# Performance work log

Hardware: AMD Instinct MI355X
Metric: run time of the kernel (lower is better)

## Reference

```python
import jax, jax.numpy as jnp
import numpy as np

KCONV = 4
NSTATE = 64
NH_SPA = 4
NH_SPE = 8
NH_ATTN = 8
QLEN = 5


def _ln(x, w, b, eps=1e-5):
    mu = jnp.mean(x, -1, keepdims=True)
    var = jnp.var(x, -1, keepdims=True)
    return (x - mu) * jax.lax.rsqrt(var + eps) * w + b


def _sincos_2d(dim, H):
    # standard 2D sin-cos positional embedding, [H*H, dim]
    def e1(d, pos):
        omega = 1.0 / (10000.0 ** (np.arange(d // 2, dtype=np.float64) / (d / 2.0)))
        out = pos[:, None] * omega[None, :]
        return np.concatenate([np.sin(out), np.cos(out)], axis=-1)
    gh, gw = np.meshgrid(np.arange(H), np.arange(H), indexing='ij')
    emb = np.concatenate([e1(dim // 2, gh.reshape(-1)), e1(dim // 2, gw.reshape(-1))], axis=-1)
    return jnp.asarray(emb, jnp.float32)


def _ssd_scan(x, dt, A, Bm, Cm):
    # x:[b,l,h,p] dt:[b,l,h] A:[h] Bm,Cm:[b,l,n] (ngroups=1)
    b, l, h, p = x.shape
    dA = jnp.exp(dt * A)            # [b,l,h]
    dtx = dt[..., None] * x          # [b,l,h,p]

    def step(hs, inp):
        dA_t, dtx_t, B_t, C_t = inp
        hs = hs * dA_t[:, :, None, None] + dtx_t[..., None] * B_t[:, None, None, :]
        return hs, jnp.einsum('bhpn,bn->bhp', hs, C_t)

    h0 = jnp.zeros((b, h, p, Bm.shape[-1]), x.dtype)
    _, ys = jax.lax.scan(step, h0, (dA.transpose(1, 0, 2), dtx.transpose(1, 0, 2, 3),
                                    Bm.transpose(1, 0, 2), Cm.transpose(1, 0, 2)))
    return ys.transpose(1, 0, 2, 3)


def _mamba2(u, in_w, conv_w, conv_b, dt_bias, A_log, Dp, rms_w, out_w, nheads, n=NSTATE):
    # Mamba2 forward (d_state=64, d_conv=4, expand=2, rmsnorm gated, no biases on projections)
    b, l, _ = u.shape
    d_in_proj = in_w.shape[0]
    d_inner = (d_in_proj - 2 * n - nheads) // 2
    zxbcdt = u @ in_w.T
    z = zxbcdt[..., :d_inner]
    xBC = zxbcdt[..., d_inner:2 * d_inner + 2 * n]
    dt = jax.nn.softplus(zxbcdt[..., 2 * d_inner + 2 * n:] + dt_bias)  # [b,l,h]
    # causal depthwise conv1d, kernel 4
    xp = jnp.pad(xBC, ((0, 0), (KCONV - 1, 0), (0, 0)))
    xc = sum(xp[:, k:k + l, :] * conv_w[:, k] for k in range(KCONV)) + conv_b
    xBC = jax.nn.silu(xc)
    xh = xBC[..., :d_inner].reshape(b, l, nheads, -1)
    Bm = xBC[..., d_inner:d_inner + n]
    Cm = xBC[..., d_inner + n:]
    y = _ssd_scan(xh, dt, -jnp.exp(A_log), Bm, Cm)
    y = y + Dp[None, None, :, None] * xh
    y = y.reshape(b, l, -1) * jax.nn.silu(z)
    y = y * jax.lax.rsqrt(jnp.mean(y * y, -1, keepdims=True) + 1e-5) * rms_w
    return y @ out_w.T


def _forward(floats, sorted_index):
    (x, spa_ln_w, spa_ln_b, spa_in_w, spa_conv_w, spa_conv_b, spa_dt_bias, spa_A_log, spa_D,
     spa_rms_w, spa_out_w, spe_ln_w, spe_ln_b, spe_in_w, spe_conv_w, spe_conv_b, spe_dt_bias,
     spe_A_log, spe_D, spe_rms_w, spe_out_w, norm_w, norm_b, cprj_w, cprj_b,
     aq_w, aq_b, ak_w, ak_b, av_w, av_b, ao_w, ao_b,
     sq_w, sq_b, sk_w, sk_b, sv_w, sv_b, so_w, so_b,
     ds_conv_w, ds_ln_w, ds_ln_b) = floats
    b, c, H, W = x.shape
    # seq_generate: pos embed + reorder by (precomputed MST/BFS) sorted_index
    pe = _sincos_2d(c, H)                                  # [H*W, c]
    xs = x.transpose(0, 2, 3, 1).reshape(b, H * W, c) + pe[None]
    xs = jnp.take_along_axis(xs, sorted_index[..., None], axis=1)
    # SSD blocks
    for i in range(spa_ln_w.shape[0]):
        h1 = _mamba2(_ln(xs, spa_ln_w[i], spa_ln_b[i]), spa_in_w[i], spa_conv_w[i], spa_conv_b[i],
                     spa_dt_bias[i], spa_A_log[i], spa_D[i], spa_rms_w[i], spa_out_w[i], NH_SPA) + xs
        h2 = _mamba2(_ln(h1.transpose(0, 2, 1), spe_ln_w[i], spe_ln_b[i]), spe_in_w[i], spe_conv_w[i],
                     spe_conv_b[i], spe_dt_bias[i], spe_A_log[i], spe_D[i], spe_rms_w[i], spe_out_w[i], NH_SPE)
        xs = h2.transpose(0, 2, 1) + h1
    xs = _ln(xs, norm_w, norm_b)
    # center query: Conv1d(kernel=QLEN, pad=0) over the first QLEN tokens -> [b, c]
    center = jnp.einsum('blc,ocl->bo', xs[:, :QLEN, :], cprj_w) + cprj_b
    # Spa_Attention: center query attends over all tokens; per-token reweighting of V
    nh = NH_ATTN
    hd = c // nh
    q = (center @ aq_w.T + aq_b).reshape(b, nh, hd)
    k = (xs @ ak_w.T + ak_b).reshape(b, -1, nh, hd)
    v = (xs @ av_w.T + av_b).reshape(b, -1, nh, hd)
    attn = jax.nn.softmax(jnp.einsum('bhd,blhd->bhl', q, k) / float(np.sqrt(hd)), axis=-1)
    out = (v * attn.transpose(0, 2, 1)[..., None]).reshape(b, -1, c) @ ao_w.T + ao_b
    xs = xs + out
    # Spe_Attention: self-attention over channel tokens (dim = seq_len)
    xt = xs.transpose(0, 2, 1)                              # [b, c, L]
    q2 = xt @ sq_w.T + sq_b
    k2 = xt @ sk_w.T + sk_b
    v2 = xt @ sv_w.T + sv_b
    attn2 = jax.nn.softmax(jnp.einsum('bqd,bkd->bqk', q2, k2) / float(np.sqrt(xt.shape[-1])), axis=-1)
    xs = xs + ((attn2 @ v2) @ so_w.T + so_b).transpose(0, 2, 1)
    # Downsample: invert ordering, reshape to image, conv stride 2, LayerNorm
    inv = jnp.argsort(sorted_index, axis=1)
    xr = jnp.take_along_axis(xs, inv[..., None], axis=1).reshape(b, H, W, c)
    y = jax.lax.conv_general_dilated(xr, ds_conv_w, (2, 2), [(1, 1), (1, 1)],
                                     dimension_numbers=('NHWC', 'HWIO', 'NHWC'))
    return _ln(y, ds_ln_w, ds_ln_b)  # [b, H/2, W/2, c]


def setup_inputs() -> dict:
    key = jax.random.key(0)
    ks = iter(jax.random.split(key, 64))

    def rn(shape, s=0.02):
        return jax.random.normal(next(ks), shape, jnp.float32) * s

    d = {}
    d['x'] = jax.random.normal(next(ks), (16, 128, 16, 16), jnp.float32)
    d['sorted_index'] = jnp.argsort(jax.random.uniform(next(ks), (16, 256)), axis=1)
    d['spa_ln_w'] = jnp.ones((2, 128), jnp.float32)
    d['spa_ln_b'] = jnp.zeros((2, 128), jnp.float32)
    d['spa_in_w'] = rn((2, 644, 128))
    d['spa_conv_w'] = rn((2, 384, 4), 0.2)
    d['spa_conv_b'] = jnp.zeros((2, 384), jnp.float32)
    d['spa_dt_bias'] = rn((2, 4), 0.1) - 2.0
    d['spa_A_log'] = jnp.log(jax.random.uniform(next(ks), (2, 4), minval=1.0, maxval=8.0))
    d['spa_D'] = jnp.ones((2, 4), jnp.float32)
    d['spa_rms_w'] = jnp.ones((2, 256), jnp.float32)
    d['spa_out_w'] = rn((2, 128, 256))
    d['spe_ln_w'] = jnp.ones((2, 256), jnp.float32)
    d['spe_ln_b'] = jnp.zeros((2, 256), jnp.float32)
    d['spe_in_w'] = rn((2, 1160, 256))
    d['spe_conv_w'] = rn((2, 640, 4), 0.2)
    d['spe_conv_b'] = jnp.zeros((2, 640), jnp.float32)
    d['spe_dt_bias'] = rn((2, 8), 0.1) - 2.0
    d['spe_A_log'] = jnp.log(jax.random.uniform(next(ks), (2, 8), minval=1.0, maxval=8.0))
    d['spe_D'] = jnp.ones((2, 8), jnp.float32)
    d['spe_rms_w'] = jnp.ones((2, 512), jnp.float32)
    d['spe_out_w'] = rn((2, 256, 512))
    d['norm_w'] = jnp.ones((128,), jnp.float32)
    d['norm_b'] = jnp.zeros((128,), jnp.float32)
    d['cprj_w'] = rn((128, 128, 5), 0.05)
    d['cprj_b'] = jnp.zeros((128,), jnp.float32)
    for nm in ['aq', 'ak', 'av', 'ao']:
        d[nm + '_w'] = rn((128, 128), 0.05)
        d[nm + '_b'] = jnp.zeros((128,), jnp.float32)
    for nm in ['sq', 'sk', 'sv', 'so']:
        d[nm + '_w'] = rn((256, 256), 0.05)
        d[nm + '_b'] = jnp.zeros((256,), jnp.float32)
    d['ds_conv_w'] = rn((3, 3, 128, 128), 0.05)
    d['ds_ln_w'] = jnp.ones((128,), jnp.float32)
    d['ds_ln_b'] = jnp.zeros((128,), jnp.float32)
    return d


def reference(x, sorted_index, spa_ln_w, spa_ln_b, spa_in_w, spa_conv_w, spa_conv_b, spa_dt_bias,
              spa_A_log, spa_D, spa_rms_w, spa_out_w, spe_ln_w, spe_ln_b, spe_in_w, spe_conv_w,
              spe_conv_b, spe_dt_bias, spe_A_log, spe_D, spe_rms_w, spe_out_w, norm_w, norm_b,
              cprj_w, cprj_b, aq_w, aq_b, ak_w, ak_b, av_w, av_b, ao_w, ao_b,
              sq_w, sq_b, sk_w, sk_b, sv_w, sv_b, so_w, so_b, ds_conv_w, ds_ln_w, ds_ln_b):
    floats = (x, spa_ln_w, spa_ln_b, spa_in_w, spa_conv_w, spa_conv_b, spa_dt_bias, spa_A_log, spa_D,
              spa_rms_w, spa_out_w, spe_ln_w, spe_ln_b, spe_in_w, spe_conv_w, spe_conv_b, spe_dt_bias,
              spe_A_log, spe_D, spe_rms_w, spe_out_w, norm_w, norm_b, cprj_w, cprj_b,
              aq_w, aq_b, ak_w, ak_b, av_w, av_b, ao_w, ao_b,
              sq_w, sq_b, sk_w, sk_b, sv_w, sv_b, so_w, so_b, ds_conv_w, ds_ln_w, ds_ln_b)
    return _forward(floats, sorted_index)
```

## Files before the change

kernel.cpp:

```cpp
#include <hip/hip_runtime.h>
#include <math.h>

#define DEV __device__ __forceinline__

typedef __attribute__((ext_vector_type(8))) short short8;
typedef __attribute__((ext_vector_type(4))) float f32x4;
typedef unsigned short ushort_t;
typedef unsigned int uint_t;

DEV float siluf(float x){ return x / (1.f + __expf(-x)); }
DEV float softplusf(float x){ return (x > 20.f) ? x : log1pf(__expf(x)); }

DEV ushort_t bf16r(float f){
    uint_t u = __float_as_uint(f);
    return (ushort_t)((u + 0x7fffu + ((u >> 16) & 1u)) >> 16);
}
DEV uint_t pack2(float a, float b){
    return (uint_t)bf16r(a) | ((uint_t)bf16r(b) << 16);
}

DEV void blk_sum2(float &a, float &b, float* sm){
    int lane = threadIdx.x & 63, wid = threadIdx.x >> 6, nw = blockDim.x >> 6;
    #pragma unroll
    for (int off = 32; off; off >>= 1){ a += __shfl_down(a, off); b += __shfl_down(b, off); }
    if (lane == 0){ sm[wid] = a; sm[8 + wid] = b; }
    __syncthreads();
    float ra = 0.f, rb = 0.f;
    for (int i = 0; i < nw; i++){ ra += sm[i]; rb += sm[8 + i]; }
    __syncthreads();
    a = ra; b = rb;
}
DEV float blk_sum1(float v, float* sm){
    int lane = threadIdx.x & 63, wid = threadIdx.x >> 6, nw = blockDim.x >> 6;
    #pragma unroll
    for (int off = 32; off; off >>= 1) v += __shfl_down(v, off);
    if (lane == 0) sm[wid] = v;
    __syncthreads();
    float r = 0.f;
    for (int i = 0; i < nw; i++) r += sm[i];
    __syncthreads();
    return r;
}
DEV float blk_max1(float v, float* sm){
    int lane = threadIdx.x & 63, wid = threadIdx.x >> 6, nw = blockDim.x >> 6;
    #pragma unroll
    for (int off = 32; off; off >>= 1) v = fmaxf(v, __shfl_down(v, off));
    if (lane == 0) sm[wid] = v;
    __syncthreads();
    float r = -3.4e38f;
    for (int i = 0; i < nw; i++) r = fmaxf(r, sm[i]);
    __syncthreads();
    return r;
}

DEV void tr_body(const float* __restrict__ ip, float* __restrict__ op,
                 int R, int C, int c0, int r0){
    __shared__ float tile[32][33];
    int tx = threadIdx.x & 31, ty = threadIdx.x >> 5;
    #pragma unroll
    for (int rr = ty; rr < 32; rr += 8)
        tile[rr][tx] = ip[(size_t)(r0 + rr) * C + c0 + tx];
    __syncthreads();
    #pragma unroll
    for (int rr = ty; rr < 32; rr += 8)
        op[(size_t)(c0 + rr) * R + r0 + tx] = tile[tx][rr];
}

__global__ __launch_bounds__(256) void k_tr(const float* __restrict__ in,
                                            float* __restrict__ out, int R, int C){
    tr_body(in + (size_t)blockIdx.z * R * C, out + (size_t)blockIdx.z * R * C,
            R, C, blockIdx.x * 32, blockIdx.y * 32);
}

__global__ __launch_bounds__(256) void k_tr_multi(const float* __restrict__ x,
        float* __restrict__ xT, const float* __restrict__ aow, float* __restrict__ owt,
        const float* __restrict__ sow, float* __restrict__ sowt){
    int idx = blockIdx.x;
    if (idx < 512){
        int bx = idx & 7, by = (idx >> 3) & 3, bz = idx >> 5;
        tr_body(x + (size_t)bz * 32768, xT + (size_t)bz * 32768, 128, 256, bx * 32, by * 32);
    } else if (idx < 528){
        int l = idx - 512;
        tr_body(aow, owt, 128, 128, (l & 3) * 32, (l >> 2) * 32);
    } else {
        int l = idx - 528;
        tr_body(sow, sowt, 256, 256, (l & 7) * 32, (l >> 3) * 32);
    }
}

__global__ void k_embed(const float* __restrict__ xT, const int* __restrict__ sidx,
                        float* __restrict__ xs){
    int bl = blockIdx.x; int b = bl >> 8; int c = threadIdx.x;
    int p = sidx[bl];
    int hh = p >> 4, ww = p & 15;
    int pos = (c < 64) ? hh : ww;
    int jm = c & 63;
    float om = __expf(-(float)(jm & 31) * 0.28782313662425574f);
    float ang = (float)pos * om;
    float pe = (jm < 32) ? sinf(ang) : cosf(ang);
    xs[(size_t)bl * 128 + c] = xT[((size_t)(b * 256 + p)) * 128 + c] + pe;
}

__global__ void k_ln(const float* __restrict__ in, const float* __restrict__ w,
                     const float* __restrict__ bb, float* __restrict__ out, int dim){
    __shared__ float sm[16];
    int row = blockIdx.x, t = threadIdx.x;
    float v = in[(size_t)row * dim + t];
    float a = v, q = v * v;
    blk_sum2(a, q, sm);
    float inv = 1.f / (float)dim;
    float mu = a * inv;
    float var = q * inv - mu * mu;
    float rs = rsqrtf(var + 1e-5f);
    out[(size_t)row * dim + t] = (v - mu) * rs * w[t] + bb[t];
}


__global__ __launch_bounds__(256) void k_gemm_ln(const float* __restrict__ A,
        const float* __restrict__ W, const float* __restrict__ lw,
        const float* __restrict__ lb, float* __restrict__ out, int N, int K){
    __shared__ __align__(16) ushort_t smem[2 * 64 * 72];
    ushort_t (*Abf)[72] = (ushort_t (*)[72])smem;
    ushort_t (*Wbf)[72] = (ushort_t (*)[72])(smem + 64 * 72);
    int j0 = blockIdx.x * 64, r0 = blockIdx.y * 64;
    int tid = threadIdx.x;
    int row = tid >> 2, kg = tid & 3;
    int wrow = j0 + row; if (wrow > N - 1) wrow = N - 1;
    const float* Ar = A + (size_t)(r0 + row) * K;
    const float* Wr = W + (size_t)wrow * K;
    float s = 0.f, ss = 0.f;
    for (int k0 = 0; k0 < K; k0 += 32){
        float4 a0 = *(const float4*)(Ar + k0 + kg * 4);
        float4 a1 = *(const float4*)(Ar + k0 + 16 + kg * 4);
        s  += a0.x + a0.y + a0.z + a0.w + a1.x + a1.y + a1.z + a1.w;
        ss += a0.x*a0.x + a0.y*a0.y + a0.z*a0.z + a0.w*a0.w
            + a1.x*a1.x + a1.y*a1.y + a1.z*a1.z + a1.w*a1.w;
    }
    s  += __shfl_xor(s, 1);  ss += __shfl_xor(ss, 1);
    s  += __shfl_xor(s, 2);  ss += __shfl_xor(ss, 2);
    float inv = 1.f / (float)K;
    float mu = s * inv;
    float rs = rsqrtf(ss * inv - mu * mu + 1e-5f);
    int wv = tid >> 6, lane = tid & 63, lm = lane & 15, quad = lane >> 4;
    f32x4 zero4 = {0.f, 0.f, 0.f, 0.f};
    f32x4 acc[4] = {zero4, zero4, zero4, zero4};
    for (int kc0 = 0; kc0 < K; kc0 += 64){
        int kb = kc0 + kg * 16;
        float4 q[4], g[4], b[4], p[4];
        #pragma unroll
        for (int i = 0; i < 4; i++){
            q[i] = *(const float4*)(Ar + kb + i * 4);
            g[i] = *(const float4*)(lw + kb + i * 4);
            b[i] = *(const float4*)(lb + kb + i * 4);
            p[i] = *(const float4*)(Wr + kb + i * 4);
        }
        #pragma unroll
        for (int i = 0; i < 4; i++){
            q[i].x = (q[i].x - mu) * rs * g[i].x + b[i].x;
            q[i].y = (q[i].y - mu) * rs * g[i].y + b[i].y;
            q[i].z = (q[i].z - mu) * rs * g[i].z + b[i].z;
            q[i].w = (q[i].w - mu) * rs * g[i].w + b[i].w;
        }
        __syncthreads();
        {
            uint4 u0, u1;
            u0.x = pack2(q[0].x, q[0].y); u0.y = pack2(q[0].z, q[0].w);
            u0.z = pack2(q[1].x, q[1].y); u0.w = pack2(q[1].z, q[1].w);
            u1.x = pack2(q[2].x, q[2].y); u1.y = pack2(q[2].z, q[2].w);
            u1.z = pack2(q[3].x, q[3].y); u1.w = pack2(q[3].z, q[3].w);
            *(uint4*)&Abf[row][kg * 16] = u0;
            *(uint4*)&Abf[row][kg * 16 + 8] = u1;
            u0.x = pack2(p[0].x, p[0].y); u0.y = pack2(p[0].z, p[0].w);
            u0.z = pack2(p[1].x, p[1].y); u0.w = pack2(p[1].z, p[1].w);
            u1.x = pack2(p[2].x, p[2].y); u1.y = pack2(p[2].z, p[2].w);
            u1.z = pack2(p[3].x, p[3].y); u1.w = pack2(p[3].z, p[3].w);
            *(uint4*)&Wbf[row][kg * 16] = u0;
            *(uint4*)&Wbf[row][kg * 16 + 8] = u1;
        }
        __syncthreads();
        #pragma unroll
        for (int kk = 0; kk < 64; kk += 32){
            short8 af = *(const short8*)&Abf[wv * 16 + lm][kk + quad * 8];
            #pragma unroll
            for (int c = 0; c < 4; c++){
                short8 bfv = *(const short8*)&Wbf[c * 16 + lm][kk + quad * 8];
                acc[c] = __builtin_amdgcn_mfma_f32_16x16x32_bf16(af, bfv, acc[c], 0, 0, 0);
            }
        }
    }
    int rbase = r0 + wv * 16 + quad * 4;
    #pragma unroll
    for (int c = 0; c < 4; c++){
        int j = j0 + c * 16 + lm;
        if (j < N){
            #pragma unroll
            for (int reg = 0; reg < 4; reg++)
                out[(size_t)(rbase + reg) * N + j] = acc[c][reg];
        }
    }
}

__global__ __launch_bounds__(256) void k_gemm_gate(const float* __restrict__ Y,
        const float* __restrict__ Z, const float* __restrict__ rw,
        const float* __restrict__ W, const float* __restrict__ res,
        float* __restrict__ out, int N, int K, int zs, int mode){
    __shared__ __align__(16) ushort_t smem[2 * 64 * 72];
    ushort_t (*Abf)[72] = (ushort_t (*)[72])smem;
    ushort_t (*Wbf)[72] = (ushort_t (*)[72])(smem + 64 * 72);
    __shared__ float sscale[64];
    int j0 = blockIdx.x * 64, r0 = blockIdx.y * 64;
    int tid = threadIdx.x;
    int row = tid >> 2, kg = tid & 3;
    const float* Yr = Y + (size_t)(r0 + row) * K;
    const float* Zr = Z + (size_t)(r0 + row) * zs;
    const float* Wr = W + (size_t)(j0 + row) * K;
    int wv = tid >> 6, lane = tid & 63, lm = lane & 15, quad = lane >> 4;
    float ssq = 0.f;
    f32x4 zero4 = {0.f, 0.f, 0.f, 0.f};
    f32x4 acc[4] = {zero4, zero4, zero4, zero4};
    for (int kc0 = 0; kc0 < K; kc0 += 64){
        int kb = kc0 + kg * 16;
        float4 y[4], z[4], g[4], p[4];
        #pragma unroll
        for (int i = 0; i < 4; i++){
            y[i] = *(const float4*)(Yr + kb + i * 4);
            z[i] = *(const float4*)(Zr + kb + i * 4);
            g[i] = *(const float4*)(rw + kb + i * 4);
            p[i] = *(const float4*)(Wr + kb + i * 4);
        }
        #pragma unroll
        for (int i = 0; i < 4; i++){
            y[i].x *= siluf(z[i].x); y[i].y *= siluf(z[i].y);
            y[i].z *= siluf(z[i].z); y[i].w *= siluf(z[i].w);
            ssq += y[i].x*y[i].x + y[i].y*y[i].y + y[i].z*y[i].z + y[i].w*y[i].w;
            y[i].x *= g[i].x; y[i].y *= g[i].y; y[i].z *= g[i].z; y[i].w *= g[i].w;
        }
        __syncthreads();
        {
            uint4 u0, u1;
            u0.x = pack2(y[0].x, y[0].y); u0.y = pack2(y[0].z, y[0].w);
            u0.z = pack2(y[1].x, y[1].y); u0.w = pack2(y[1].z, y[1].w);
            u1.x = pack2(y[2].x, y[2].y); u1.y = pack2(y[2].z, y[2].w);
            u1.z = pack2(y[3].x, y[3].y); u1.w = pack2(y[3].z, y[3].w);
            *(uint4*)&Abf[row][kg * 16] = u0;
            *(uint4*)&Abf[row][kg * 16 + 8] = u1;
            u0.x = pack2(p[0].x, p[0].y); u0.y = pack2(p[0].z, p[0].w);
            u0.z = pack2(p[1].x, p[1].y); u0.w = pack2(p[1].z, p[1].w);
            u1.x = pack2(p[2].x, p[2].y); u1.y = pack2(p[2].z, p[2].w);
            u1.z = pack2(p[3].x, p[3].y); u1.w = pack2(p[3].z, p[3].w);
            *(uint4*)&Wbf[row][kg * 16] = u0;
            *(uint4*)&Wbf[row][kg * 16 + 8] = u1;
        }
        __syncthreads();
        #pragma unroll
        for (int kk = 0; kk < 64; kk += 32){
            short8 af = *(const short8*)&Abf[wv * 16 + lm][kk + quad * 8];
            #pragma unroll
            for (int c = 0; c < 4; c++){
                short8 bfv = *(const short8*)&Wbf[c * 16 + lm][kk + quad * 8];
                acc[c] = __builtin_amdgcn_mfma_f32_16x16x32_bf16(af, bfv, acc[c], 0, 0, 0);
            }
        }
    }
    ssq += __shfl_xor(ssq, 1);
    ssq += __shfl_xor(ssq, 2);
    if (kg == 0) sscale[row] = rsqrtf(ssq / (float)K + 1e-5f);
    __syncthreads();
    int lr0 = wv * 16 + quad * 4;
    float scr[4];
    #pragma unroll
    for (int reg = 0; reg < 4; reg++) scr[reg] = sscale[lr0 + reg];
    if (mode == 2){
        float (*T)[68] = (float (*)[68])smem;
        #pragma unroll
        for (int c = 0; c < 4; c++)
            #pragma unroll
            for (int reg = 0; reg < 4; reg++)
                T[c * 16 + lm][lr0 + reg] = acc[c][reg] * scr[reg];
        __syncthreads();
        int b2 = r0 >> 7, ii0 = r0 & 127;
        int jj = tid >> 2, seg = tid & 3;
        size_t base = ((size_t)(b2 * 256 + j0 + jj)) * 128 + ii0 + seg * 16;
        float* op = out + base;
        const float* rp = res + base;
        #pragma unroll
        for (int c = 0; c < 4; c++){
            float4 v = *(const float4*)(&T[jj][seg * 16 + c * 4]);
            float4 rv = *(const float4*)(rp + c * 4);
            v.x += rv.x; v.y += rv.y; v.z += rv.z; v.w += rv.w;
            *(float4*)(op + c * 4) = v;
        }
    } else {
        int rbase = r0 + lr0;
        #pragma unroll
        for (int c = 0; c < 4; c++){
            int j = j0 + c * 16 + lm;
            #pragma unroll
            for (int reg = 0; reg < 4; reg++){
                size_t oi = (size_t)(rbase + reg) * N + j;
                out[oi] = acc[c][reg] * scr[reg] + res[oi];
            }
        }
    }
}

struct GJob { const float* W; const float* bias; float* out; int mode; };

__global__ __launch_bounds__(256) void k_gemm3(const float* __restrict__ A,
                                               GJob ja, GJob jb, GJob jc,
                                               int N, int K){
    GJob job = (blockIdx.z == 0) ? ja : ((blockIdx.z == 1) ? jb : jc);
    const float* W = job.W;
    const float* bias = job.bias;
    float* out = job.out;
    int mode = job.mode;
    __shared__ __align__(16) ushort_t smem[2 * 64 * 72];
    ushort_t (*Abf)[72] = (ushort_t (*)[72])smem;
    ushort_t (*Wbf)[72] = (ushort_t (*)[72])(smem + 64 * 72);
    int j0 = blockIdx.x * 64, r0 = blockIdx.y * 64;
    int tid = threadIdx.x;
    int row = tid >> 2, kg = tid & 3;
    const float* Ar = A + (size_t)(r0 + row) * K;
    const float* Wr = W + (size_t)(j0 + row) * K;
    int wv = tid >> 6, lane = tid & 63, lm = lane & 15, quad = lane >> 4;
    f32x4 zero4 = {0.f, 0.f, 0.f, 0.f};
    f32x4 acc[4] = {zero4, zero4, zero4, zero4};
    for (int kc0 = 0; kc0 < K; kc0 += 64){
        int kb = kc0 + kg * 16;
        float4 q[4], p[4];
        #pragma unroll
        for (int i = 0; i < 4; i++){
            q[i] = *(const float4*)(Ar + kb + i * 4);
            p[i] = *(const float4*)(Wr + kb + i * 4);
        }
        __syncthreads();
        {
            uint4 u0, u1;
            u0.x = pack2(q[0].x, q[0].y); u0.y = pack2(q[0].z, q[0].w);
            u0.z = pack2(q[1].x, q[1].y); u0.w = pack2(q[1].z, q[1].w);
            u1.x = pack2(q[2].x, q[2].y); u1.y = pack2(q[2].z, q[2].w);
            u1.z = pack2(q[3].x, q[3].y); u1.w = pack2(q[3].z, q[3].w);
            *(uint4*)&Abf[row][kg * 16] = u0;
            *(uint4*)&Abf[row][kg * 16 + 8] = u1;
            u0.x = pack2(p[0].x, p[0].y); u0.y = pack2(p[0].z, p[0].w);
            u0.z = pack2(p[1].x, p[1].y); u0.w = pack2(p[1].z, p[1].w);
            u1.x = pack2(p[2].x, p[2].y); u1.y = pack2(p[2].z, p[2].w);
            u1.z = pack2(p[3].x, p[3].y); u1.w = pack2(p[3].z, p[3].w);
            *(uint4*)&Wbf[row][kg * 16] = u0;
            *(uint4*)&Wbf[row][kg * 16 + 8] = u1;
        }
        __syncthreads();
        #pragma unroll
        for (int kk = 0; kk < 64; kk += 32){
            short8 af = *(const short8*)&Abf[wv * 16 + lm][kk + quad * 8];
            #pragma unroll
            for (int c = 0; c < 4; c++){
                short8 bfv = *(const short8*)&Wbf[c * 16 + lm][kk + quad * 8];
                acc[c] = __builtin_amdgcn_mfma_f32_16x16x32_bf16(af, bfv, acc[c], 0, 0, 0);
            }
        }
    }
    int lr0 = wv * 16 + quad * 4;
    if (mode == 3){
        __syncthreads();
        float (*T)[68] = (float (*)[68])smem;
        #pragma unroll
        for (int c = 0; c < 4; c++)
            #pragma unroll
            for (int reg = 0; reg < 4; reg++)
                T[c * 16 + lm][lr0 + reg] = acc[c][reg];
        __syncthreads();
        int b2 = r0 >> 7, ii0 = r0 & 127;
        int jj = tid >> 2, seg = tid & 3;
        size_t base = ((size_t)(b2 * 256 + j0 + jj)) * 128 + ii0 + seg * 16;
        float* op = out + base;
        float bj = bias[j0 + jj];
        #pragma unroll
        for (int c = 0; c < 4; c++){
            float4 v = *(const float4*)(&T[jj][seg * 16 + c * 4]);
            v.x += bj; v.y += bj; v.z += bj; v.w += bj;
            *(float4*)(op + c * 4) = v;
        }
    } else {
        int rbase = r0 + lr0;
        #pragma unroll
        for (int c = 0; c < 4; c++){
            int j = j0 + c * 16 + lm;
            float bj = bias[j];
            #pragma unroll
            for (int reg = 0; reg < 4; reg++)
                out[(size_t)(rbase + reg) * N + j] = acc[c][reg] + bj;
        }
    }
}

__global__ void k_conv(const float* __restrict__ zx, const float* __restrict__ cw,
                       const float* __restrict__ cb, float* __restrict__ xc,
                       const float* __restrict__ dtbias, const float* __restrict__ Al,
                       float* __restrict__ dt, float* __restrict__ dlA,
                       int L, int D, int stride, int off, int nh, int dtoff){
    int bl = blockIdx.x;
    int l = bl & (L - 1);
    const float* base = zx + (size_t)bl * stride + off;
    for (int d = threadIdx.x; d < D; d += blockDim.x){
        float acc = cb[d];
        #pragma unroll
        for (int k = 0; k < 4; k++){
            int dl = l + k - 3;
            if (dl >= 0) acc += base[(ptrdiff_t)(k - 3) * stride + d] * cw[d * 4 + k];
        }
        xc[(size_t)bl * D + d] = siluf(acc);
    }
    int t = threadIdx.x;
    if (t < nh){
        float xv = zx[(size_t)bl * stride + dtoff + t] + dtbias[t];
        float d = softplusf(xv);
        dt[(size_t)bl * nh + t] = d;
        dlA[(size_t)bl * nh + t] = -d * __expf(Al[t]);
    }
}

__global__ __launch_bounds__(256) void k_ssd_chunk(
        const float* __restrict__ xc, const float* __restrict__ dt,
        const float* __restrict__ dlA, float* __restrict__ y,
        float* __restrict__ S, float* __restrict__ clb,
        int L, int nh, int nc, int xcs, int bo, int co, int ys){
    __shared__ float sX[64][68];
    __shared__ float sB[64][68];
    __shared__ float sC[64][68];
    __shared__ float cl[64], sdt[64], sw[64];
    int blk = blockIdx.x;
    int c = blk % nc; int bh = blk / nc; int h = bh % nh; int b = bh / nh;
    int l0 = c * 64;
    int tid = threadIdx.x;
    const float* base = xc + ((size_t)(b * L + l0)) * xcs;
    for (int idx = tid; idx < 4096; idx += 256){
        int s = idx >> 6, n = idx & 63;
        const float* row = base + (size_t)s * xcs;
        sX[s][n] = row[h * 64 + n];
        sB[s][n] = row[bo + n];
        sC[s][n] = row[co + n];
    }
    if (tid < 64){
        size_t di = (size_t)(b * L + l0 + tid) * nh + h;
        float dlv = dlA[di];
        sdt[tid] = dt[di];
        #pragma unroll
        for (int off = 1; off < 64; off <<= 1){
            float o = __shfl_up(dlv, off, 64);
            if (tid >= off) dlv += o;
        }
        cl[tid] = dlv;
        clb[(size_t)blk * 64 + tid] = dlv;
    }
    __syncthreads();
    if (tid < 64) sw[tid] = __expf(cl[63] - cl[tid]) * sdt[tid];

    int g1 = tid >> 4, g2 = tid & 15;
    int t0 = g1 * 4, s0 = g2 * 4;
    float g[4][4] = {};
    for (int n = 0; n < 64; n += 4){
        float4 cv[4], bv[4];
        #pragma unroll
        for (int i = 0; i < 4; i++) cv[i] = *(const float4*)&sC[t0 + i][n];
        #pragma unroll
        for (int j = 0; j < 4; j++) bv[j] = *(const float4*)&sB[s0 + j][n];
        #pragma unroll
        for (int i = 0; i < 4; i++)
            #pragma unroll
            for (int j = 0; j < 4; j++){
                g[i][j] = fmaf(cv[i].x, bv[j].x, g[i][j]);
                g[i][j] = fmaf(cv[i].y, bv[j].y, g[i][j]);
                g[i][j] = fmaf(cv[i].z, bv[j].z, g[i][j]);
                g[i][j] = fmaf(cv[i].w, bv[j].w, g[i][j]);
            }
    }
    __syncthreads();
    #pragma unroll
    for (int i = 0; i < 4; i++)
        #pragma unroll
        for (int j = 0; j < 4; j++){
            int t = t0 + i, s = s0 + j;
            float v = 0.f;
            if (s <= t) v = g[i][j] * __expf(cl[t] - cl[s]) * sdt[s];
            sC[t][s] = v;
        }
    __syncthreads();
    {
        float acc[4][4] = {};
        for (int s = 0; s < 64; s++){
            float4 xv = *(const float4*)&sX[s][s0];
            float gv[4];
            #pragma unroll
            for (int i = 0; i < 4; i++) gv[i] = sC[t0 + i][s];
            #pragma unroll
            for (int i = 0; i < 4; i++){
                acc[i][0] = fmaf(gv[i], xv.x, acc[i][0]);
                acc[i][1] = fmaf(gv[i], xv.y, acc[i][1]);
                acc[i][2] = fmaf(gv[i], xv.z, acc[i][2]);
                acc[i][3] = fmaf(gv[i], xv.w, acc[i][3]);
            }
        }
        #pragma unroll
        for (int i = 0; i < 4; i++){
            float4 o = make_float4(acc[i][0], acc[i][1], acc[i][2], acc[i][3]);
            *(float4*)&y[(size_t)(b * L + l0 + t0 + i) * ys + h * 64 + s0] = o;
        }
    }
    {
        float acc[4][4] = {};
        int p0 = t0, n0 = s0;
        for (int s = 0; s < 64; s++){
            float wv = sw[s];
            float4 bv = *(const float4*)&sB[s][n0];
            float4 xv = *(const float4*)&sX[s][p0];
            float w0 = wv * xv.x, w1 = wv * xv.y, w2 = wv * xv.z, w3 = wv * xv.w;
            acc[0][0] = fmaf(w0, bv.x, acc[0][0]); acc[0][1] = fmaf(w0, bv.y, acc[0][1]);
            acc[0][2] = fmaf(w0, bv.z, acc[0][2]); acc[0][3] = fmaf(w0, bv.w, acc[0][3]);
            acc[1][0] = fmaf(w1, bv.x, acc[1][0]); acc[1][1] = fmaf(w1, bv.y, acc[1][1]);
            acc[1][2] = fmaf(w1, bv.z, acc[1][2]); acc[1][3] = fmaf(w1, bv.w, acc[1][3]);
            acc[2][0] = fmaf(w2, bv.x, acc[2][0]); acc[2][1] = fmaf(w2, bv.y, acc[2][1]);
            acc[2][2] = fmaf(w2, bv.z, acc[2][2]); acc[2][3] = fmaf(w2, bv.w, acc[2][3]);
            acc[3][0] = fmaf(w3, bv.x, acc[3][0]); acc[3][1] = fmaf(w3, bv.y, acc[3][1]);
            acc[3][2] = fmaf(w3, bv.z, acc[3][2]); acc[3][3] = fmaf(w3, bv.w, acc[3][3]);
        }
        float* Sp = S + (size_t)blk * 4096;
        #pragma unroll
        for (int i = 0; i < 4; i++){
            float4 o = make_float4(acc[i][0], acc[i][1], acc[i][2], acc[i][3]);
            *(float4*)&Sp[(p0 + i) * 64 + n0] = o;
        }
    }
}

__global__ __launch_bounds__(256) void k_chunk_y(
        const float* __restrict__ xc, const float* __restrict__ S,
        const float* __restrict__ clb, const float* __restrict__ Dp,
        float* __restrict__ y,
        int L, int nh, int nc, int xcs, int co, int ys){
    __shared__ float sH[64][68];
    __shared__ float sC[64][68];
    __shared__ float scl[64];
    int blk = blockIdx.x;
    int c = blk % nc; int bh = blk / nc; int h = bh % nh; int b = bh / nh;
    int l0 = c * 64;
    int tid = threadIdx.x;
    float wch[4];
    {
        float w = 1.f;
        for (int cp = c - 1; cp >= 0; cp--){
            wch[cp] = w;
            w *= __expf(clb[((size_t)(bh * nc + cp)) * 64 + 63]);
        }
    }
    const float* Sb = S + (size_t)(bh * nc) * 4096;
    const float* base = xc + ((size_t)(b * L + l0)) * xcs;
    for (int idx = tid; idx < 4096; idx += 256){
        int r = idx >> 6, n = idx & 63;
        float hv = 0.f;
        for (int cp = 0; cp < c; cp++)
            hv = fmaf(wch[cp], Sb[(size_t)cp * 4096 + idx], hv);
        sH[r][n] = hv;
        sC[r][n] = base[(size_t)r * xcs + co + n];
    }
    if (tid < 64) scl[tid] = __expf(clb[(size_t)blk * 64 + tid]);
    float Dh = Dp[h];
    __syncthreads();
    int g1 = tid >> 4, g2 = tid & 15;
    int t0 = g1 * 4, p0 = g2 * 4;
    float m[4][4] = {};
    for (int n = 0; n < 64; n += 4){
        float4 cv[4], hv[4];
        #pragma unroll
        for (int i = 0; i < 4; i++) cv[i] = *(const float4*)&sC[t0 + i][n];
        #pragma unroll
        for (int j = 0; j < 4; j++) hv[j] = *(const float4*)&sH[p0 + j][n];
        #pragma unroll
        for (int i = 0; i < 4; i++)
            #pragma unroll
            for (int j = 0; j < 4; j++){
                m[i][j] = fmaf(cv[i].x, hv[j].x, m[i][j]);
                m[i][j] = fmaf(cv[i].y, hv[j].y, m[i][j]);
                m[i][j] = fmaf(cv[i].z, hv[j].z, m[i][j]);
                m[i][j] = fmaf(cv[i].w, hv[j].w, m[i][j]);
            }
    }
    #pragma unroll
    for (int i = 0; i < 4; i++){
        int t = t0 + i;
        size_t yi = (size_t)(b * L + l0 + t) * ys + h * 64 + p0;
        float4 yv = *(float4*)&y[yi];
        float4 xv = *(const float4*)&base[(size_t)t * xcs + h * 64 + p0];
        float e = scl[t];
        yv.x += e * m[i][0] + Dh * xv.x;
        yv.y += e * m[i][1] + Dh * xv.y;
        yv.z += e * m[i][2] + Dh * xv.z;
        yv.w += e * m[i][3] + Dh * xv.w;
        *(float4*)&y[yi] = yv;
    }
}

__global__ void k_center_q(const float* __restrict__ xs, const float* __restrict__ cw,
                           const float* __restrict__ cb, const float* __restrict__ qw,
                           const float* __restrict__ qb, float* __restrict__ q){
    __shared__ float xr[640];
    __shared__ float cen[128];
    int b = blockIdx.x, t = threadIdx.x;
    for (int idx = t; idx < 640; idx += 128)
        xr[idx] = xs[(size_t)b * 256 * 128 + idx];
    __syncthreads();
    float acc = cb[t];
    for (int c = 0; c < 128; c++){
        const float* wp = cw + (size_t)(t * 128 + c) * 5;
        #pragma unroll
        for (int l = 0; l < 5; l++) acc += xr[l * 128 + c] * wp[l];
    }
    cen[t] = acc;
    __syncthreads();
    float qa = qb[t];
    const float* wr = qw + (size_t)t * 128;
    for (int o = 0; o < 128; o++) qa += cen[o] * wr[o];
    q[b * 128 + t] = qa;
}

__global__ void k_attn(const float* __restrict__ q, const float* __restrict__ k,
                       float* __restrict__ attn){
    __shared__ float sm[16];
    __shared__ float qh[16];
    int blk = blockIdx.x; int b = blk >> 3, h = blk & 7; int l = threadIdx.x;
    if (l < 16) qh[l] = q[b * 128 + h * 16 + l];
    __syncthreads();
    const float* kp = k + ((size_t)(b * 256 + l)) * 128 + h * 16;
    float s = 0.f;
    #pragma unroll
    for (int d = 0; d < 16; d++) s += qh[d] * kp[d];
    s *= 0.25f;
    float mx = blk_max1(s, sm);
    float e = __expf(s - mx);
    float sum = blk_sum1(e, sm);
    attn[(size_t)blk * 256 + l] = e / sum;
}

__global__ __launch_bounds__(128) void k_attn_out(const float* __restrict__ v,
                                                  const float* __restrict__ attn,
                                                  const float* __restrict__ owt,
                                                  const float* __restrict__ ob,
                                                  float* __restrict__ xs){
    __shared__ float vp[8][128];
    int blk = blockIdx.x; int b = blk >> 5, l0 = (blk & 31) << 3;
    int t = threadIdx.x;
    int h = t >> 4;
    float a[8];
    #pragma unroll
    for (int r = 0; r < 8; r++)
        a[r] = attn[((size_t)(b * 8 + h)) * 256 + l0 + r];
    #pragma unroll
    for (int r = 0; r < 8; r++)
        vp[r][t] = v[((size_t)(b * 256 + l0 + r)) * 128 + t] * a[r];
    __syncthreads();
    float acc[8];
    float bv = ob[t];
    #pragma unroll
    for (int r = 0; r < 8; r++) acc[r] = bv;
    for (int j = 0; j < 128; j++){
        float w = owt[j * 128 + t];
        #pragma unroll
        for (int r = 0; r < 8; r++) acc[r] = fmaf(vp[r][j], w, acc[r]);
    }
    #pragma unroll
    for (int r = 0; r < 8; r++)
        xs[((size_t)(b * 256 + l0 + r)) * 128 + t] += acc[r];
}

__global__ __launch_bounds__(256) void k_spe_attn(const float* __restrict__ q2,
        const float* __restrict__ k2t, const float* __restrict__ v2,
        const float* __restrict__ sowt, const float* __restrict__ sob,
        const float* __restrict__ xs, const int* __restrict__ sidx,
        float* __restrict__ xr){
    __shared__ float qs[8][256];
    __shared__ float lgp[2][8][128];
    __shared__ float sa[8][132];
    __shared__ float av[8][256];
    __shared__ float mxs[8], sms[8];
    int blk = blockIdx.x; int b = blk >> 4; int i0 = (blk & 15) << 3;
    int t = threadIdx.x;
    for (int idx = t; idx < 2048; idx += 256){
        int ii = idx >> 8, d = idx & 255;
        qs[ii][d] = q2[((size_t)(b * 128 + i0 + ii)) * 256 + d];
    }
    __syncthreads();
    {
        int j = t & 127, dh = t >> 7;
        const float* kt = k2t + (size_t)b * 32768 + dh * 16384;
        float acc[8] = {};
        for (int dd = 0; dd < 128; dd++){
            float kv = kt[dd * 128 + j];
            int d = dh * 128 + dd;
            #pragma unroll
            for (int ii = 0; ii < 8; ii++) acc[ii] = fmaf(qs[ii][d], kv, acc[ii]);
        }
        #pragma unroll
        for (int ii = 0; ii < 8; ii++) lgp[dh][ii][j] = acc[ii];
    }
    __syncthreads();
    if (t < 128){
        #pragma unroll
        for (int ii = 0; ii < 8; ii++)
            sa[ii][t] = (lgp[0][ii][t] + lgp[1][ii][t]) * (1.f / 16.f);
    }
    __syncthreads();
    if (t < 8){
        float mx = -3.4e38f;
        for (int j = 0; j < 128; j++) mx = fmaxf(mx, sa[t][j]);
        float sm = 0.f;
        for (int j = 0; j < 128; j++) sm += __expf(sa[t][j] - mx);
        mxs[t] = mx; sms[t] = 1.f / sm;
    }
    __syncthreads();
    if (t < 128){
        #pragma unroll
        for (int ii = 0; ii < 8; ii++)
            sa[ii][t] = __expf(sa[ii][t] - mxs[ii]) * sms[ii];
    }
    __syncthreads();
    {
        float acc[8] = {};
        const float* vb = v2 + (size_t)b * 32768 + t;
        for (int j = 0; j < 128; j++){
            float vv = vb[(size_t)j * 256];
            #pragma unroll
            for (int ii = 0; ii < 8; ii++) acc[ii] = fmaf(sa[ii][j], vv, acc[ii]);
        }
        #pragma unroll
        for (int ii = 0; ii < 8; ii++) av[ii][t] = acc[ii];
    }
    __syncthreads();
    float acc[8] = {};
    for (int d = 0; d < 256; d++){
        float wv = sowt[d * 256 + t];
        #pragma unroll
        for (int ii = 0; ii < 8; ii++) acc[ii] = fmaf(av[ii][d], wv, acc[ii]);
    }
    float bias = sob[t];
    int p = sidx[b * 256 + t];
    const float* xin = xs + ((size_t)(b * 256 + t)) * 128 + i0;
    float* xout = xr + ((size_t)(b * 256 + p)) * 128 + i0;
    #pragma unroll
    for (int ii = 0; ii < 8; ii++) xout[ii] = xin[ii] + acc[ii] + bias;
}

__global__ __launch_bounds__(256) void k_conv_gemm(const float* __restrict__ xr,
                                                   const float* __restrict__ W2,
                                                   float* __restrict__ part){
    __shared__ float As[16][68];
    __shared__ float Ws[16][64];
    int j0 = blockIdx.x * 64, r0 = blockIdx.y * 64, s = blockIdx.z;
    int tid = threadIdx.x;
    int cg = tid & 15, rg = tid >> 4;
    int arow = tid >> 2, akg = tid & 3;
    int wkk = tid >> 4, wseg = tid & 15;
    int r = r0 + arow; int b = r >> 6, oh = (r >> 3) & 7, ow = r & 7;
    float acc[4][4] = {};
    int kbeg = s * 288, kend = kbeg + 288;
    float4 a4, w4;
    {
        int k = kbeg + akg * 4;
        int khw = k >> 7, c = k & 127;
        int kh = khw / 3, kw = khw - kh * 3;
        int ih = oh * 2 - 1 + kh, iw = ow * 2 - 1 + kw;
        a4 = make_float4(0.f, 0.f, 0.f, 0.f);
        if (ih >= 0 && ih < 16 && iw >= 0 && iw < 16)
            a4 = *(const float4*)(xr + ((size_t)((b << 8) + (ih << 4) + iw)) * 128 + c);
        w4 = *(const float4*)(W2 + (size_t)(kbeg + wkk) * 128 + j0 + wseg * 4);
    }
    for (int k0 = kbeg; k0 < kend; k0 += 16){
        __syncthreads();
        As[akg * 4 + 0][arow] = a4.x; As[akg * 4 + 1][arow] = a4.y;
        As[akg * 4 + 2][arow] = a4.z; As[akg * 4 + 3][arow] = a4.w;
        Ws[wkk][wseg * 4 + 0] = w4.x; Ws[wkk][wseg * 4 + 1] = w4.y;
        Ws[wkk][wseg * 4 + 2] = w4.z; Ws[wkk][wseg * 4 + 3] = w4.w;
        __syncthreads();
        bool more = (k0 + 16 < kend);
        float4 na4, nw4;
        if (more){
            int k = k0 + 16 + akg * 4;
            int khw = k >> 7, c = k & 127;
            int kh = khw / 3, kw = khw - kh * 3;
            int ih = oh * 2 - 1 + kh, iw = ow * 2 - 1 + kw;
            na4 = make_float4(0.f, 0.f, 0.f, 0.f);
            if (ih >= 0 && ih < 16 && iw >= 0 && iw < 16)
                na4 = *(const float4*)(xr + ((size_t)((b << 8) + (ih << 4) + iw)) * 128 + c);
            nw4 = *(const float4*)(W2 + (size_t)(k0 + 16 + wkk) * 128 + j0 + wseg * 4);
        }
        #pragma unroll
        for (int kk = 0; kk < 16; kk++){
            float4 av4 = *(const float4*)(&As[kk][rg << 2]);
            float4 wv4 = *(const float4*)(&Ws[kk][cg << 2]);
            float av_[4] = {av4.x, av4.y, av4.z, av4.w};
            float wv_[4] = {wv4.x, wv4.y, wv4.z, wv4.w};
            #pragma unroll
            for (int ri = 0; ri < 4; ri++)
                #pragma unroll
                for (int ci = 0; ci < 4; ci++)
                    acc[ri][ci] = fmaf(av_[ri], wv_[ci], acc[ri][ci]);
        }
        if (more){ a4 = na4; w4 = nw4; }
    }
    float* pp = part + (size_t)s * 1024 * 128;
    #pragma unroll
    for (int ri = 0; ri < 4; ri++){
        int rr = r0 + (rg << 2) + ri;
        #pragma unroll
        for (int ci = 0; ci < 4; ci++){
            int j = j0 + (cg << 2) + ci;
            pp[(size_t)rr * 128 + j] = acc[ri][ci];
        }
    }
}

__global__ void k_part_ln(const float* __restrict__ part, const float* __restrict__ lnw,
                          const float* __restrict__ lnb, float* __restrict__ out){
    __shared__ float sm[16];
    int r = blockIdx.x, t = threadIdx.x;
    float v = part[(size_t)r * 128 + t]
            + part[(size_t)(1024 + r) * 128 + t]
            + part[(size_t)(2048 + r) * 128 + t]
            + part[(size_t)(3072 + r) * 128 + t];
    float a = v, q = v * v;
    blk_sum2(a, q, sm);
    float mu = a * (1.f / 128.f);
    float var = q * (1.f / 128.f) - mu * mu;
    float rs = rsqrtf(var + 1e-5f);
    out[(size_t)r * 128 + t] = (v - mu) * rs * lnw[t] + lnb[t];
}

extern "C" void kernel_launch(void* const* d_in, const int* in_sizes, int n_in,
                              void* d_out, int out_size, void* d_ws, size_t ws_size,
                              hipStream_t stream) {
    const float* x          = (const float*)d_in[0];
    const int*   sidx       = (const int*)  d_in[1];
    const float* spa_ln_w   = (const float*)d_in[2];
    const float* spa_ln_b   = (const float*)d_in[3];
    const float* spa_in_w   = (const float*)d_in[4];
    const float* spa_conv_w = (const float*)d_in[5];
    const float* spa_conv_b = (const float*)d_in[6];
    const float* spa_dt_bias= (const float*)d_in[7];
    const float* spa_A_log  = (const float*)d_in[8];
    const float* spa_D      = (const float*)d_in[9];
    const float* spa_rms_w  = (const float*)d_in[10];
    const float* spa_out_w  = (const float*)d_in[11];
    const float* spe_ln_w   = (const float*)d_in[12];
    const float* spe_ln_b   = (const float*)d_in[13];
    const float* spe_in_w   = (const float*)d_in[14];
    const float* spe_conv_w = (const float*)d_in[15];
    const float* spe_conv_b = (const float*)d_in[16];
    const float* spe_dt_bias= (const float*)d_in[17];
    const float* spe_A_log  = (const float*)d_in[18];
    const float* spe_D      = (const float*)d_in[19];
    const float* spe_rms_w  = (const float*)d_in[20];
    const float* spe_out_w  = (const float*)d_in[21];
    const float* norm_w     = (const float*)d_in[22];
    const float* norm_b     = (const float*)d_in[23];
    const float* cprj_w     = (const float*)d_in[24];
    const float* cprj_b     = (const float*)d_in[25];
    const float* aq_w       = (const float*)d_in[26];
    const float* aq_b       = (const float*)d_in[27];
    const float* ak_w       = (const float*)d_in[28];
    const float* ak_b       = (const float*)d_in[29];
    const float* av_w       = (const float*)d_in[30];
    const float* av_b       = (const float*)d_in[31];
    const float* ao_w       = (const float*)d_in[32];
    const float* ao_b       = (const float*)d_in[33];
    const float* sq_w       = (const float*)d_in[34];
    const float* sq_b       = (const float*)d_in[35];
    const float* sk_w       = (const float*)d_in[36];
    const float* sk_b       = (const float*)d_in[37];
    const float* sv_w       = (const float*)d_in[38];
    const float* sv_b       = (const float*)d_in[39];
    const float* so_w       = (const float*)d_in[40];
    const float* so_b       = (const float*)d_in[41];
    const float* ds_conv_w  = (const float*)d_in[42];
    const float* ds_ln_w    = (const float*)d_in[43];
    const float* ds_ln_b    = (const float*)d_in[44];

    float* ws = (float*)d_ws;
    float* xs   = ws + 0;
    float* zx   = ws + 1048576;
    float* xc   = ws + 3686400;
    float* dtb  = ws + 5259264;
    float* dAb  = ws + 5292032;
    float* yb   = ws + 5324800;
    float* Sbuf = ws + 6373376;
    float* h1   = ws + 7421952;
    float* clbuf = ws + 524288;
    float* xT    = ws + 524288;
    float* h1t   = ws + 6373376;
    float* owt   = ws + 7946240;
    float* sowt  = ws + 7962624;
    float* kb    = ws + 1048576;
    float* vb    = ws + 1572864;
    float* attnb = ws + 2097152;
    float* qb    = ws + 2129920;
    float* xt    = ws + 524288;
    float* q2    = ws + 3686400;
    float* k2t   = ws + 4210688;
    float* v2    = ws + 4734976;
    float* xr    = ws + 5586944;
    float* part  = ws + 1048576;

    k_tr_multi<<<592, 256, 0, stream>>>(x, xT, ao_w, owt, so_w, sowt);
    k_embed<<<4096, 128, 0, stream>>>(xT, sidx, xs);

    for (int i = 0; i < 2; i++){
        k_gemm_ln<<<dim3(11, 64), 256, 0, stream>>>(xs, spa_in_w + (size_t)i * 644 * 128,
                                                    spa_ln_w + i * 128, spa_ln_b + i * 128,
                                                    zx, 644, 128);
        k_conv<<<4096, 256, 0, stream>>>(zx, spa_conv_w + (size_t)i * 384 * 4,
                                         spa_conv_b + i * 384, xc,
                                         spa_dt_bias + i * 4, spa_A_log + i * 4, dtb, dAb,
                                         256, 384, 644, 256, 4, 640);
        k_ssd_chunk<<<256, 256, 0, stream>>>(xc, dtb, dAb, yb, Sbuf, clbuf,
                                             256, 4, 4, 384, 256, 320, 256);
        k_chunk_y<<<256, 256, 0, stream>>>(xc, Sbuf, clbuf, spa_D + i * 4, yb,
                                           256, 4, 4, 384, 320, 256);
        k_gemm_gate<<<dim3(2, 64), 256, 0, stream>>>(yb, zx, spa_rms_w + i * 256,
                                                     spa_out_w + (size_t)i * 128 * 256,
                                                     xs, h1, 128, 256, 644, 1);
        k_tr<<<dim3(4, 8, 16), 256, 0, stream>>>(h1, h1t, 256, 128);
        k_gemm_ln<<<dim3(19, 32), 256, 0, stream>>>(h1t, spe_in_w + (size_t)i * 1160 * 256,
                                                    spe_ln_w + i * 256, spe_ln_b + i * 256,
                                                    zx, 1160, 256);
        k_conv<<<2048, 256, 0, stream>>>(zx, spe_conv_w + (size_t)i * 640 * 4,
                                         spe_conv_b + i * 640, xc,
                                         spe_dt_bias + i * 8, spe_A_log + i * 8, dtb, dAb,
                                         128, 640, 1160, 512, 8, 1152);
        k_ssd_chunk<<<256, 256, 0, stream>>>(xc, dtb, dAb, yb, Sbuf, clbuf,
                                             128, 8, 2, 640, 512, 576, 512);
        k_chunk_y<<<256, 256, 0, stream>>>(xc, Sbuf, clbuf, spe_D + i * 8, yb,
                                           128, 8, 2, 640, 576, 512);
        k_gemm_gate<<<dim3(4, 32), 256, 0, stream>>>(yb, zx, spe_rms_w + i * 512,
                                                     spe_out_w + (size_t)i * 256 * 512,
                                                     h1, xs, 256, 512, 1160, 2);
    }

    k_ln<<<4096, 128, 0, stream>>>(xs, norm_w, norm_b, xs, 128);
    k_center_q<<<16, 128, 0, stream>>>(xs, cprj_w, cprj_b, aq_w, aq_b, qb);
    {
        GJob jk = {ak_w, ak_b, kb, 0};
        GJob jv = {av_w, av_b, vb, 0};
        k_gemm3<<<dim3(2, 64, 2), 256, 0, stream>>>(xs, jk, jv, jk, 128, 128);
    }
    k_attn<<<128, 256, 0, stream>>>(qb, kb, attnb);
    k_attn_out<<<512, 128, 0, stream>>>(vb, attnb, owt, ao_b, xs);
    k_tr<<<dim3(4, 8, 16), 256, 0, stream>>>(xs, xt, 256, 128);
    {
        GJob jq = {sq_w, sq_b, q2, 0};
        GJob jk = {sk_w, sk_b, k2t, 3};
        GJob jv = {sv_w, sv_b, v2, 0};
        k_gemm3<<<dim3(4, 32, 3), 256, 0, stream>>>(xt, jq, jk, jv, 256, 256);
    }
    k_spe_attn<<<256, 256, 0, stream>>>(q2, k2t, v2, sowt, so_b, xs, sidx, xr);
    k_conv_gemm<<<dim3(2, 16, 4), 256, 0, stream>>>(xr, ds_conv_w, part);
    k_part_ln<<<1024, 128, 0, stream>>>(part, ds_ln_w, ds_ln_b, (float*)d_out);
}
```

Before: 549.0 us.

## Fuse causal conv and dt softplus into SSD kernels; fuse transpose into out-proj

Drops the separate depthwise conv/softplus kernel. The conv, SiLU and dt/dA computation are now recomputed inside the chunk-scan and chunk-output kernels straight from the in-projection buffer, so the xc/dt/dA intermediates are never written to or read from memory. The out-projection GEMM gains a mode that also writes a transposed copy through shared memory, which removes the standalone transpose launch. The cost is redundant conv work, since B/C and X are recomputed by each head block and by both kernels, and the reads from the wide zx rows are strided.

Measured after the change: 615.2 us. 1.12x slower.

```diff
diff --git a/kernel.cpp b/kernel.cpp
--- a/kernel.cpp
+++ b/kernel.cpp
@@ -203,7 +203,8 @@
 __global__ __launch_bounds__(256) void k_gemm_gate(const float* __restrict__ Y,
         const float* __restrict__ Z, const float* __restrict__ rw,
         const float* __restrict__ W, const float* __restrict__ res,
-        float* __restrict__ out, int N, int K, int zs, int mode){
+        float* __restrict__ out, float* __restrict__ out2,
+        int N, int K, int zs, int mode){
     __shared__ __align__(16) ushort_t smem[2 * 64 * 72];
     ushort_t (*Abf)[72] = (ushort_t (*)[72])smem;
     ushort_t (*Wbf)[72] = (ushort_t (*)[72])(smem + 64 * 72);
@@ -291,6 +292,7 @@
             *(float4*)(op + c * 4) = v;
         }
     } else {
+        float (*T)[68] = (float (*)[68])smem;
         int rbase = r0 + lr0;
         #pragma unroll
         for (int c = 0; c < 4; c++){
@@ -298,7 +300,21 @@
             #pragma unroll
             for (int reg = 0; reg < 4; reg++){
                 size_t oi = (size_t)(rbase + reg) * N + j;
-                out[oi] = acc[c][reg] * scr[reg] + res[oi];
+                float v = acc[c][reg] * scr[reg] + res[oi];
+                out[oi] = v;
+                if (mode == 4) T[c * 16 + lm][lr0 + reg] = v;
+            }
+        }
+        if (mode == 4){
+            __syncthreads();
+            int bb = r0 >> 8, lbase = r0 & 255;
+            int jj = tid >> 2, seg = tid & 3;
+            size_t base2 = ((size_t)(bb * 128 + j0 + jj)) * 256 + lbase + seg * 16;
+            float* op = out2 + base2;
+            #pragma unroll
+            for (int cc = 0; cc < 4; cc++){
+                float4 v = *(const float4*)(&T[jj][seg * 16 + cc * 4]);
+                *(float4*)(op + cc * 4) = v;
             }
         }
     }
@@ -394,37 +410,13 @@
     }
 }
 
-__global__ void k_conv(const float* __restrict__ zx, const float* __restrict__ cw,
-                       const float* __restrict__ cb, float* __restrict__ xc,
-                       const float* __restrict__ dtbias, const float* __restrict__ Al,
-                       float* __restrict__ dt, float* __restrict__ dlA,
-                       int L, int D, int stride, int off, int nh, int dtoff){
-    int bl = blockIdx.x;
-    int l = bl & (L - 1);
-    const float* base = zx + (size_t)bl * stride + off;
-    for (int d = threadIdx.x; d < D; d += blockDim.x){
-        float acc = cb[d];
-        #pragma unroll
-        for (int k = 0; k < 4; k++){
-            int dl = l + k - 3;
-            if (dl >= 0) acc += base[(ptrdiff_t)(k - 3) * stride + d] * cw[d * 4 + k];
-        }
-        xc[(size_t)bl * D + d] = siluf(acc);
-    }
-    int t = threadIdx.x;
-    if (t < nh){
-        float xv = zx[(size_t)bl * stride + dtoff + t] + dtbias[t];
-        float d = softplusf(xv);
-        dt[(size_t)bl * nh + t] = d;
-        dlA[(size_t)bl * nh + t] = -d * __expf(Al[t]);
-    }
-}
-
 __global__ __launch_bounds__(256) void k_ssd_chunk(
-        const float* __restrict__ xc, const float* __restrict__ dt,
-        const float* __restrict__ dlA, float* __restrict__ y,
+        const float* __restrict__ zx, const float* __restrict__ cw,
+        const float* __restrict__ cb, const float* __restrict__ dtbias,
+        const float* __restrict__ Al, float* __restrict__ y,
         float* __restrict__ S, float* __restrict__ clb,
-        int L, int nh, int nc, int xcs, int bo, int co, int ys){
+        int L, int nh, int nc, int zxs, int zoff, int bo, int co,
+        int dtcol, int ys){
     __shared__ float sX[64][68];
     __shared__ float sB[64][68];
     __shared__ float sC[64][68];
@@ -433,18 +425,35 @@
     int c = blk % nc; int bh = blk / nc; int h = bh % nh; int b = bh / nh;
     int l0 = c * 64;
     int tid = threadIdx.x;
-    const float* base = xc + ((size_t)(b * L + l0)) * xcs;
+    const float* zb = zx + (size_t)(b * L) * zxs + zoff;
     for (int idx = tid; idx < 4096; idx += 256){
         int s = idx >> 6, n = idx & 63;
-        const float* row = base + (size_t)s * xcs;
-        sX[s][n] = row[h * 64 + n];
-        sB[s][n] = row[bo + n];
-        sC[s][n] = row[co + n];
+        int l = l0 + s;
+        int d0 = h * 64 + n, d1 = bo + n, d2 = co + n;
+        float a0 = cb[d0], a1 = cb[d1], a2 = cb[d2];
+        float4 w0 = *(const float4*)(cw + d0 * 4);
+        float4 w1 = *(const float4*)(cw + d1 * 4);
+        float4 w2 = *(const float4*)(cw + d2 * 4);
+        #pragma unroll
+        for (int k = 0; k < 4; k++){
+            int dl = l + k - 3;
+            if (dl >= 0){
+                const float* zr = zb + (size_t)dl * zxs;
+                a0 += zr[d0] * (&w0.x)[k];
+                a1 += zr[d1] * (&w1.x)[k];
+                a2 += zr[d2] * (&w2.x)[k];
+            }
+        }
+        sX[s][n] = siluf(a0);
+        sB[s][n] = siluf(a1);
+        sC[s][n] = siluf(a2);
     }
     if (tid < 64){
-        size_t di = (size_t)(b * L + l0 + tid) * nh + h;
-        float dlv = dlA[di];
-        sdt[tid] = dt[di];
+        int l = l0 + tid;
+        float xv = zx[((size_t)(b * L + l)) * zxs + dtcol + h] + dtbias[h];
+        float dtv = softplusf(xv);
+        float dlv = -dtv * __expf(Al[h]);
+        sdt[tid] = dtv;
         #pragma unroll
         for (int off = 1; off < 64; off <<= 1){
             float o = __shfl_up(dlv, off, 64);
@@ -534,12 +543,14 @@
 }
 
 __global__ __launch_bounds__(256) void k_chunk_y(
-        const float* __restrict__ xc, const float* __restrict__ S,
+        const float* __restrict__ zx, const float* __restrict__ cw,
+        const float* __restrict__ cb, const float* __restrict__ S,
         const float* __restrict__ clb, const float* __restrict__ Dp,
         float* __restrict__ y,
-        int L, int nh, int nc, int xcs, int co, int ys){
+        int L, int nh, int nc, int zxs, int zoff, int co, int ys){
     __shared__ float sH[64][68];
     __shared__ float sC[64][68];
+    __shared__ float sXc[64][68];
     __shared__ float scl[64];
     int blk = blockIdx.x;
     int c = blk % nc; int bh = blk / nc; int h = bh % nh; int b = bh / nh;
@@ -554,14 +565,29 @@
         }
     }
     const float* Sb = S + (size_t)(bh * nc) * 4096;
-    const float* base = xc + ((size_t)(b * L + l0)) * xcs;
+    const float* zb = zx + (size_t)(b * L) * zxs + zoff;
     for (int idx = tid; idx < 4096; idx += 256){
         int r = idx >> 6, n = idx & 63;
+        int l = l0 + r;
         float hv = 0.f;
         for (int cp = 0; cp < c; cp++)
             hv = fmaf(wch[cp], Sb[(size_t)cp * 4096 + idx], hv);
         sH[r][n] = hv;
-        sC[r][n] = base[(size_t)r * xcs + co + n];
+        int d0 = h * 64 + n, d2 = co + n;
+        float a0 = cb[d0], a2 = cb[d2];
+        float4 w0 = *(const float4*)(cw + d0 * 4);
+        float4 w2 = *(const float4*)(cw + d2 * 4);
+        #pragma unroll
+        for (int k = 0; k < 4; k++){
+            int dl = l + k - 3;
+            if (dl >= 0){
+                const float* zr = zb + (size_t)dl * zxs;
+                a0 += zr[d0] * (&w0.x)[k];
+                a2 += zr[d2] * (&w2.x)[k];
+            }
+        }
+        sXc[r][n] = siluf(a0);
+        sC[r][n] = siluf(a2);
     }
     if (tid < 64) scl[tid] = __expf(clb[(size_t)blk * 64 + tid]);
     float Dh = Dp[h];
@@ -590,7 +616,7 @@
         int t = t0 + i;
         size_t yi = (size_t)(b * L + l0 + t) * ys + h * 64 + p0;
         float4 yv = *(float4*)&y[yi];
-        float4 xv = *(const float4*)&base[(size_t)t * xcs + h * 64 + p0];
+        float4 xv = *(const float4*)&sXc[t][p0];
         float e = scl[t];
         yv.x += e * m[i][0] + Dh * xv.x;
         yv.y += e * m[i][1] + Dh * xv.y;
@@ -886,9 +912,6 @@
     float* ws = (float*)d_ws;
     float* xs   = ws + 0;
     float* zx   = ws + 1048576;
-    float* xc   = ws + 3686400;
-    float* dtb  = ws + 5259264;
-    float* dAb  = ws + 5292032;
     float* yb   = ws + 5324800;
     float* Sbuf = ws + 6373376;
     float* h1   = ws + 7421952;
@@ -915,32 +938,31 @@
         k_gemm_ln<<<dim3(11, 64), 256, 0, stream>>>(xs, spa_in_w + (size_t)i * 644 * 128,
                                                     spa_ln_w + i * 128, spa_ln_b + i * 128,
                                                     zx, 644, 128);
-        k_conv<<<4096, 256, 0, stream>>>(zx, spa_conv_w + (size_t)i * 384 * 4,
-                                         spa_conv_b + i * 384, xc,
-                                         spa_dt_bias + i * 4, spa_A_log + i * 4, dtb, dAb,
-                                         256, 384, 644, 256, 4, 640);
-        k_ssd_chunk<<<256, 256, 0, stream>>>(xc, dtb, dAb, yb, Sbuf, clbuf,
-                                             256, 4, 4, 384, 256, 320, 256);
-        k_chunk_y<<<256, 256, 0, stream>>>(xc, Sbuf, clbuf, spa_D + i * 4, yb,
-                                           256, 4, 4, 384, 320, 256);
+        k_ssd_chunk<<<256, 256, 0, stream>>>(zx, spa_conv_w + (size_t)i * 384 * 4,
+                                             spa_conv_b + i * 384, spa_dt_bias + i * 4,
+                                             spa_A_log + i * 4, yb, Sbuf, clbuf,
+                                             256, 4, 4, 644, 256, 256, 320, 640, 256);
+        k_chunk_y<<<256, 256, 0, stream>>>(zx, spa_conv_w + (size_t)i * 384 * 4,
+                                           spa_conv_b + i * 384, Sbuf, clbuf,
+                                           spa_D + i * 4, yb,
+                                           256, 4, 4, 644, 256, 320, 256);
         k_gemm_gate<<<dim3(2, 64), 256, 0, stream>>>(yb, zx, spa_rms_w + i * 256,
                                                      spa_out_w + (size_t)i * 128 * 256,
-                                                     xs, h1, 128, 256, 644, 1);
-        k_tr<<<dim3(4, 8, 16), 256, 0, stream>>>(h1, h1t, 256, 128);
+                                                     xs, h1, h1t, 128, 256, 644, 4);
         k_gemm_ln<<<dim3(19, 32), 256, 0, stream>>>(h1t, spe_in_w + (size_t)i * 1160 * 256,
                                                     spe_ln_w + i * 256, spe_ln_b + i * 256,
                                                     zx, 1160, 256);
-        k_conv<<<2048, 256, 0, stream>>>(zx, spe_conv_w + (size_t)i * 640 * 4,
-                                         spe_conv_b + i * 640, xc,
-                                         spe_dt_bias + i * 8, spe_A_log + i * 8, dtb, dAb,
-                                         128, 640, 1160, 512, 8, 1152);
-        k_ssd_chunk<<<256, 256, 0, stream>>>(xc, dtb, dAb, yb, Sbuf, clbuf,
-                                             128, 8, 2, 640, 512, 576, 512);
-        k_chunk_y<<<256, 256, 0, stream>>>(xc, Sbuf, clbuf, spe_D + i * 8, yb,
-                                           128, 8, 2, 640, 576, 512);
+        k_ssd_chunk<<<256, 256, 0, stream>>>(zx, spe_conv_w + (size_t)i * 640 * 4,
+                                             spe_conv_b + i * 640, spe_dt_bias + i * 8,
+                                             spe_A_log + i * 8, yb, Sbuf, clbuf,
+                                             128, 8, 2, 1160, 512, 512, 576, 1152, 512);
+        k_chunk_y<<<256, 256, 0, stream>>>(zx, spe_conv_w + (size_t)i * 640 * 4,
+                                           spe_conv_b + i * 640, Sbuf, clbuf,
+                                           spe_D + i * 8, yb,
+                                           128, 8, 2, 1160, 512, 576, 512);
         k_gemm_gate<<<dim3(4, 32), 256, 0, stream>>>(yb, zx, spe_rms_w + i * 512,
                                                      spe_out_w + (size_t)i * 256 * 512,
-                                                     h1, xs, 256, 512, 1160, 2);
+                                                     h1, xs, nullptr, 256, 512, 1160, 2);
     }
 
     k_ln<<<4096, 128, 0, stream>>>(xs, norm_w, norm_b, xs, 128);
```
